# Kernel tuning notes

Hardware: AMD Instinct MI355X
Metric: run time of the kernel (lower is better)

Reference implementation:

```python
import jax, jax.numpy as jnp
import numpy as np

D_MODEL = 1024
N_HEADS = 16
HEAD_DIM = D_MODEL // N_HEADS


def setup_inputs() -> dict:
    key = jax.random.key(0)
    ks = jax.random.split(key, 9)
    s = 1.0 / np.sqrt(D_MODEL)
    inp = {
        "x": jax.random.normal(ks[0], (4, 2048, D_MODEL), dtype=jnp.float32),
        "wq": jax.random.uniform(ks[1], (D_MODEL, D_MODEL), jnp.float32, -s, s),
        "bq": jax.random.uniform(ks[2], (D_MODEL,), jnp.float32, -s, s),
        "wk": jax.random.uniform(ks[3], (D_MODEL, D_MODEL), jnp.float32, -s, s),
        "bk": jax.random.uniform(ks[4], (D_MODEL,), jnp.float32, -s, s),
        "wv": jax.random.uniform(ks[5], (D_MODEL, D_MODEL), jnp.float32, -s, s),
        "bv": jax.random.uniform(ks[6], (D_MODEL,), jnp.float32, -s, s),
        "wo": jax.random.uniform(ks[7], (D_MODEL, D_MODEL), jnp.float32, -s, s),
        "bo": jax.random.uniform(ks[8], (D_MODEL,), jnp.float32, -s, s),
    }
    return inp


def reference(x, wq, bq, wk, bk, wv, bv, wo, bo):
    b, s, d = x.shape
    h, hd = N_HEADS, HEAD_DIM
    # projections (torch Linear: y = x @ W.T + b; here weights stored as [in, out])
    q = (x @ wq + bq).reshape(b, s, h, hd).transpose(0, 2, 1, 3)  # [b,h,s,hd]
    k = (x @ wk + bk).reshape(b, s, h, hd).transpose(0, 2, 1, 3)
    v = (x @ wv + bv).reshape(b, s, h, hd).transpose(0, 2, 1, 3)
    scores = jnp.einsum("bhqd,bhkd->bhqk", q, k) / jnp.sqrt(jnp.float32(hd))
    causal = jnp.tril(jnp.ones((s, s), dtype=bool))
    scores = jnp.where(causal, scores, -jnp.inf)
    weights = jax.nn.softmax(scores, axis=-1)
    attn = jnp.einsum("bhqk,bhkd->bhqd", weights, v)  # [b,h,s,hd]
    attn = attn.transpose(0, 2, 1, 3).reshape(b, s, d)
    return attn @ wo + bo
```

## Files before the change

kernel.cpp:

```cpp
#include <hip/hip_runtime.h>
#include <cstddef>

#define D_MODEL 1024
#define NH 16
#define HD 64
#define BATCH 4
#define SEQ 2048
#define MTOT (BATCH * SEQ)

typedef _Float16 half8 __attribute__((ext_vector_type(8)));
typedef _Float16 half4v __attribute__((ext_vector_type(4)));
typedef float f32x4 __attribute__((ext_vector_type(4)));

#if __has_builtin(__builtin_amdgcn_exp2f)
#define EXP2(x) __builtin_amdgcn_exp2f(x)
#else
#define EXP2(x) __expf((x)*0.69314718056f)
#endif

#define ASYNC_COPY16(g, l)                                                    \
    __builtin_amdgcn_global_load_lds(                                         \
        (__attribute__((address_space(1))) const void*)(g),                   \
        (__attribute__((address_space(3))) void*)(l), 16, 0, 0)

#define LDSFRAG(S, R, CH)                                                     \
    (*(const half8*)((const char*)(S) + ((R) << 7) +                          \
                     ((((CH) << 1)) ^ (((R) & 7) << 4))))
#define LDSWADDR(S, R, CH)                                                    \
    ((half8*)((char*)(S) + ((R) << 7) + ((((CH) << 1)) ^ (((R) & 7) << 4))))

__global__ __launch_bounds__(256) void prep(
    const float* __restrict__ x, _Float16* __restrict__ xh,
    const float* __restrict__ W0, const float* __restrict__ W1,
    const float* __restrict__ W2, const float* __restrict__ W3,
    _Float16* __restrict__ T0, _Float16* __restrict__ T1,
    _Float16* __restrict__ T2, _Float16* __restrict__ T3)
{
    __shared__ float T[64][65];
    const int bid = blockIdx.x;
    if (bid < 256) {
        const size_t base = (size_t)bid * 4096 + threadIdx.x;
#pragma unroll
        for (int it = 0; it < 16; ++it) {
            const size_t i = base + (size_t)it * 256;
            const float4* p = (const float4*)x + 2 * i;
            float4 a = p[0], b = p[1];
            half8 h;
            h[0] = (_Float16)a.x; h[1] = (_Float16)a.y; h[2] = (_Float16)a.z; h[3] = (_Float16)a.w;
            h[4] = (_Float16)b.x; h[5] = (_Float16)b.y; h[6] = (_Float16)b.z; h[7] = (_Float16)b.w;
            *((half8*)xh + i) = h;
        }
    } else {
        const int t = bid - 256;
        const int mtx = t >> 8;
        const float* W = (mtx == 0) ? W0 : (mtx == 1) ? W1 : (mtx == 2) ? W2 : W3;
        _Float16*   Wt = (mtx == 0) ? T0 : (mtx == 1) ? T1 : (mtx == 2) ? T2 : T3;
        const int tile = t & 255;
        const int k0 = (tile >> 4) * 64, n0 = (tile & 15) * 64;
        const int r = threadIdx.x >> 4, c4 = (threadIdx.x & 15) * 4;

#pragma unroll
        for (int i = 0; i < 4; ++i) {
            float4 v = *(const float4*)(W + (size_t)(k0 + r + 16 * i) * 1024 + n0 + c4);
            T[r + 16 * i][c4 + 0] = v.x; T[r + 16 * i][c4 + 1] = v.y;
            T[r + 16 * i][c4 + 2] = v.z; T[r + 16 * i][c4 + 3] = v.w;
        }
        __syncthreads();
#pragma unroll
        for (int i = 0; i < 4; ++i) {
            const int n = r + 16 * i;
            half4v h;
            h[0] = (_Float16)T[c4 + 0][n]; h[1] = (_Float16)T[c4 + 1][n];
            h[2] = (_Float16)T[c4 + 2][n]; h[3] = (_Float16)T[c4 + 3][n];
            *(half4v*)(Wt + (size_t)(n0 + n) * 1024 + k0 + c4) = h;
        }
    }
}

template <int QKV>
__global__ __launch_bounds__(256) void gemm_mfma(
    const _Float16* __restrict__ A,
    const _Float16* __restrict__ Bt0, const _Float16* __restrict__ Bt1, const _Float16* __restrict__ Bt2,
    const float* __restrict__ bi0, const float* __restrict__ bi1, const float* __restrict__ bi2,
    void* __restrict__ C0, void* __restrict__ C1, void* __restrict__ C2)
{
    const int L = blockIdx.x;
    const int y = L & 63;
    const int c_ = L >> 6;
    const int z  = QKV ? (c_ >> 3) : 0;
    const int xb = QKV ? (c_ & 7) : c_;

    const _Float16* Bt = (z == 0) ? Bt0 : (z == 1) ? Bt1 : Bt2;
    const float*   bia = (z == 0) ? bi0 : (z == 1) ? bi1 : bi2;
    void*            C = (z == 0) ? C0  : (z == 1) ? C1  : C2;

    __shared__ _Float16 As[128][64];
    __shared__ _Float16 Bs[128][64];

    const int tid  = threadIdx.x;
    const int w    = tid >> 6;
    const int lane = tid & 63;
    const int l15  = lane & 15;
    const int lg   = lane >> 4;
    const int m0 = y * 128;
    const int n0 = xb * 128;
    const int wm = (w >> 1) * 64, wn = (w & 1) * 64;

    const int rsub = lane >> 3;
    const int cswz = ((lane & 7) ^ rsub) * 8;

    const _Float16* gA = A  + (size_t)(m0 + 32 * w + rsub) * 1024 + cswz;
    const _Float16* gB = Bt + (size_t)(n0 + 32 * w + rsub) * 1024 + cswz;
    char* lA = (char*)As + (size_t)(w * 4) * 1024;
    char* lB = (char*)Bs + (size_t)(w * 4) * 1024;

    f32x4 acc[4][4];
#pragma unroll
    for (int i = 0; i < 4; ++i)
#pragma unroll
        for (int j = 0; j < 4; ++j) { acc[i][j][0] = 0.f; acc[i][j][1] = 0.f; acc[i][j][2] = 0.f; acc[i][j][3] = 0.f; }

    for (int kt = 0; kt < 16; ++kt) {
        const int k0 = kt * 64;
        __syncthreads();
#pragma unroll
        for (int i = 0; i < 4; ++i) {
            ASYNC_COPY16(gA + (size_t)(8 * i) * 1024 + k0, lA + i * 1024);
            ASYNC_COPY16(gB + (size_t)(8 * i) * 1024 + k0, lB + i * 1024);
        }
        __syncthreads();

#pragma unroll
        for (int c = 0; c < 2; ++c) {
            half8 af[4], bf[4];
#pragma unroll
            for (int i = 0; i < 4; ++i) af[i] = LDSFRAG(As, wm + 16 * i + l15, 32 * c + 8 * lg);
#pragma unroll
            for (int j = 0; j < 4; ++j) bf[j] = LDSFRAG(Bs, wn + 16 * j + l15, 32 * c + 8 * lg);
#pragma unroll
            for (int i = 0; i < 4; ++i)
#pragma unroll
                for (int j = 0; j < 4; ++j)
                    acc[i][j] = __builtin_amdgcn_mfma_f32_16x16x32_f16(af[i], bf[j], acc[i][j], 0, 0, 0);
        }
    }

    float bvv[4];
#pragma unroll
    for (int j = 0; j < 4; ++j) bvv[j] = bia[n0 + wn + 16 * j + l15];

#pragma unroll
    for (int i = 0; i < 4; ++i)
#pragma unroll
        for (int j = 0; j < 4; ++j)
#pragma unroll
            for (int r = 0; r < 4; ++r) {
                const int m = m0 + wm + 16 * i + 4 * lg + r;
                const int n = n0 + wn + 16 * j + l15;
                const float val = acc[i][j][r] + bvv[j];
                if (QKV) {
                    const int bb = m >> 11, ss = m & 2047, hh = n >> 6, hd = n & 63;
                    if (z < 2)
                        ((_Float16*)C)[((size_t)(bb * NH + hh) * SEQ + ss) * HD + hd] = (_Float16)val;
                    else
                        ((_Float16*)C)[((size_t)(bb * NH + hh) * HD + hd) * SEQ + ss] = (_Float16)val;
                } else {
                    ((float*)C)[(size_t)m * 1024 + n] = val;
                }
            }
}

__global__ __launch_bounds__(256, 6) void attn_fwd_mfma(
    const _Float16* __restrict__ Q, const _Float16* __restrict__ K,
    const _Float16* __restrict__ Vt, _Float16* __restrict__ O)
{
    __shared__ _Float16 Ks[64][64];
    __shared__ _Float16 Vs[64][64];
    __shared__ _Float16 Ps[4][16][72];

    const int tid  = threadIdx.x;
    const int w    = tid >> 6;
    const int lane = tid & 63;
    const int l15  = lane & 15;
    const int lg   = lane >> 4;

    const int bid = blockIdx.x;
    const int bh  = bid & 63;
    const int qtb = bid >> 6;
    const int b  = bh >> 4, h = bh & 15;

    const _Float16* Qb  = Q  + (size_t)bh * SEQ * HD;
    const _Float16* Kb  = K  + (size_t)bh * SEQ * HD;
    const _Float16* Vtb = Vt + (size_t)bh * HD * SEQ;

    const int srow = tid >> 3;
    const int scol = (tid & 7) * 8;

    for (int pass = 0; pass < 2; ++pass) {
        const int qt = pass ? qtb : (31 - qtb);
        const int q0 = qt * 64;
        const int ntiles = qt + 1;

        half8 qa[2];
        {
            const _Float16* qp = Qb + (size_t)(q0 + 16 * w + l15) * HD + 8 * lg;
            qa[0] = *(const half8*)(qp);
            qa[1] = *(const half8*)(qp + 32);
#pragma unroll
            for (int c = 0; c < 2; ++c)
#pragma unroll
                for (int j = 0; j < 8; ++j)
                    qa[c][j] = (_Float16)((float)qa[c][j] * 0.18033688f);
        }

        f32x4 o_[4];
#pragma unroll
        for (int ft = 0; ft < 4; ++ft) { o_[ft][0] = 0.f; o_[ft][1] = 0.f; o_[ft][2] = 0.f; o_[ft][3] = 0.f; }
        float lp_t = 0.f;

        half8 kreg[2], vreg[2];
#pragma unroll
        for (int j = 0; j < 2; ++j) {
            kreg[j] = *(const half8*)(Kb  + (size_t)(srow + 32 * j) * HD + scol);
            vreg[j] = *(const half8*)(Vtb + (size_t)(srow + 32 * j) * SEQ + scol);
        }

        for (int kt = 0; kt < ntiles; ++kt) {
            __syncthreads();
#pragma unroll
            for (int j = 0; j < 2; ++j) {
                const int row = srow + 32 * j;
                *LDSWADDR(Ks, row, scol) = kreg[j];
                *LDSWADDR(Vs, row, scol) = vreg[j];
            }
            __syncthreads();

            if (kt + 1 < ntiles) {
                const int k0 = (kt + 1) * 64;
#pragma unroll
                for (int j = 0; j < 2; ++j) {
                    kreg[j] = *(const half8*)(Kb  + (size_t)(k0 + srow + 32 * j) * HD + scol);
                    vreg[j] = *(const half8*)(Vtb + (size_t)(srow + 32 * j) * SEQ + k0 + scol);
                }
            }

            f32x4 s[4];
#pragma unroll
            for (int f = 0; f < 4; ++f) { s[f][0] = 0.f; s[f][1] = 0.f; s[f][2] = 0.f; s[f][3] = 0.f; }
#pragma unroll
            for (int c = 0; c < 2; ++c)
#pragma unroll
                for (int f = 0; f < 4; ++f) {
                    half8 kb = LDSFRAG(Ks, 16 * f + l15, 32 * c + 8 * lg);
                    s[f] = __builtin_amdgcn_mfma_f32_16x16x32_f16(kb, qa[c], s[f], 0, 0, 0);
                }

            const bool dg = (kt == qt);
#pragma unroll
            for (int f = 0; f < 4; ++f) {
                half4v ph;
#pragma unroll
                for (int r = 0; r < 4; ++r) {
                    float p = EXP2(s[f][r]);
                    if (dg && (16 * f + 4 * lg + r > 16 * w + l15)) p = 0.f;
                    lp_t += p;
                    ph[r] = (_Float16)p;
                }
                *(half4v*)&Ps[w][l15][16 * f + 4 * lg] = ph;
            }

            half8 pa[2];
            pa[0] = *(const half8*)&Ps[w][l15][8 * lg];
            pa[1] = *(const half8*)&Ps[w][l15][32 + 8 * lg];
#pragma unroll
            for (int c = 0; c < 2; ++c)
#pragma unroll
                for (int ft = 0; ft < 4; ++ft) {
                    half8 vb = LDSFRAG(Vs, 16 * ft + l15, 32 * c + 8 * lg);
                    o_[ft] = __builtin_amdgcn_mfma_f32_16x16x32_f16(pa[c], vb, o_[ft], 0, 0, 0);
                }
        }

        float rs = lp_t;
        rs += __shfl_xor(rs, 16);
        rs += __shfl_xor(rs, 32);
#pragma unroll
        for (int r = 0; r < 4; ++r) {
            const float inv = 1.0f / __shfl(rs, 4 * lg + r, 64);
            _Float16* orow = O + (size_t)(b * SEQ + q0 + 16 * w + 4 * lg + r) * D_MODEL + h * HD + l15;
#pragma unroll
            for (int ft = 0; ft < 4; ++ft) orow[16 * ft] = (_Float16)(o_[ft][r] * inv);
        }
        __syncthreads();
    }
}

extern "C" void kernel_launch(void* const* d_in, const int* in_sizes, int n_in,
                              void* d_out, int out_size, void* d_ws, size_t ws_size,
                              hipStream_t stream)
{
    const float* x  = (const float*)d_in[0];
    const float* wq = (const float*)d_in[1];
    const float* bq = (const float*)d_in[2];
    const float* wk = (const float*)d_in[3];
    const float* bk = (const float*)d_in[4];
    const float* wv = (const float*)d_in[5];
    const float* bv = (const float*)d_in[6];
    const float* wo = (const float*)d_in[7];
    const float* bo = (const float*)d_in[8];
    float* out = (float*)d_out;

    const size_t SZ = (size_t)MTOT * D_MODEL;
    const size_t WZ = (size_t)D_MODEL * D_MODEL;

    _Float16* xh  = (_Float16*)d_ws;
    _Float16* wtq = xh + SZ;
    _Float16* wtk = wtq + WZ;
    _Float16* wtv = wtk + WZ;
    _Float16* wto = wtv + WZ;
    _Float16* Qh  = wto + WZ;
    _Float16* Kh  = Qh + SZ;
    _Float16* Vtg = Kh + SZ;
    _Float16* AOh = Vtg + SZ;

    prep<<<dim3(1280), 256, 0, stream>>>(x, xh, wq, wk, wv, wo, wtq, wtk, wtv, wto);
    gemm_mfma<1><<<dim3(1536), 256, 0, stream>>>(xh, wtq, wtk, wtv, bq, bk, bv, Qh, Kh, Vtg);
    attn_fwd_mfma<<<dim3(1024), 256, 0, stream>>>(Qh, Kh, Vtg, AOh);
    gemm_mfma<0><<<dim3(512), 256, 0, stream>>>(AOh, wto, wto, wto, bo, bo, bo, out, out, out);
}
```

Measured before the change: 268.9 us.

## Double attention query tile to 128 rows per block for K/V reuse

Each attention block now processes 128 query rows (two 16-row sub-tiles per wave) instead of 64, so every K/V tile loaded into LDS is reused by twice as many queries. The grid is halved to 512 blocks and launch bounds lowered to 4 to accommodate doubled accumulator registers. This reduces K/V global/LDS traffic and syncs per query but lowers occupancy, halves the number of blocks, and adds wasted masked work on the two diagonal tiles.

```diff
diff --git a/kernel.cpp b/kernel.cpp
--- a/kernel.cpp
+++ b/kernel.cpp
@@ -170,13 +170,13 @@
             }
 }
 
-__global__ __launch_bounds__(256, 6) void attn_fwd_mfma(
+__global__ __launch_bounds__(256, 4) void attn_fwd_mfma(
     const _Float16* __restrict__ Q, const _Float16* __restrict__ K,
     const _Float16* __restrict__ Vt, _Float16* __restrict__ O)
 {
     __shared__ _Float16 Ks[64][64];
     __shared__ _Float16 Vs[64][64];
-    __shared__ _Float16 Ps[4][16][72];
+    __shared__ _Float16 Ps[8][16][72];
 
     const int tid  = threadIdx.x;
     const int w    = tid >> 6;
@@ -197,26 +197,29 @@
     const int scol = (tid & 7) * 8;
 
     for (int pass = 0; pass < 2; ++pass) {
-        const int qt = pass ? qtb : (31 - qtb);
-        const int q0 = qt * 64;
-        const int ntiles = qt + 1;
-
-        half8 qa[2];
-        {
-            const _Float16* qp = Qb + (size_t)(q0 + 16 * w + l15) * HD + 8 * lg;
-            qa[0] = *(const half8*)(qp);
-            qa[1] = *(const half8*)(qp + 32);
+        const int qt = pass ? qtb : (15 - qtb);
+        const int q0 = qt * 128;
+        const int ntiles = 2 * qt + 2;
+
+        half8 qa[2][2];
+#pragma unroll
+        for (int u = 0; u < 2; ++u) {
+            const _Float16* qp = Qb + (size_t)(q0 + 16 * (2 * w + u) + l15) * HD + 8 * lg;
+            qa[u][0] = *(const half8*)(qp);
+            qa[u][1] = *(const half8*)(qp + 32);
 #pragma unroll
             for (int c = 0; c < 2; ++c)
 #pragma unroll
                 for (int j = 0; j < 8; ++j)
-                    qa[c][j] = (_Float16)((float)qa[c][j] * 0.18033688f);
-        }
-
-        f32x4 o_[4];
-#pragma unroll
-        for (int ft = 0; ft < 4; ++ft) { o_[ft][0] = 0.f; o_[ft][1] = 0.f; o_[ft][2] = 0.f; o_[ft][3] = 0.f; }
-        float lp_t = 0.f;
+                    qa[u][c][j] = (_Float16)((float)qa[u][c][j] * 0.18033688f);
+        }
+
+        f32x4 o_[2][4];
+#pragma unroll
+        for (int u = 0; u < 2; ++u)
+#pragma unroll
+            for (int ft = 0; ft < 4; ++ft) { o_[u][ft][0] = 0.f; o_[u][ft][1] = 0.f; o_[u][ft][2] = 0.f; o_[u][ft][3] = 0.f; }
+        float lp_t[2] = {0.f, 0.f};
 
         half8 kreg[2], vreg[2];
 #pragma unroll
@@ -244,52 +247,67 @@
                 }
             }
 
-            f32x4 s[4];
-#pragma unroll
-            for (int f = 0; f < 4; ++f) { s[f][0] = 0.f; s[f][1] = 0.f; s[f][2] = 0.f; s[f][3] = 0.f; }
+            f32x4 s0[4], s1[4];
+#pragma unroll
+            for (int f = 0; f < 4; ++f) {
+                s0[f][0] = 0.f; s0[f][1] = 0.f; s0[f][2] = 0.f; s0[f][3] = 0.f;
+                s1[f][0] = 0.f; s1[f][1] = 0.f; s1[f][2] = 0.f; s1[f][3] = 0.f;
+            }
 #pragma unroll
             for (int c = 0; c < 2; ++c)
 #pragma unroll
                 for (int f = 0; f < 4; ++f) {
                     half8 kb = LDSFRAG(Ks, 16 * f + l15, 32 * c + 8 * lg);
-                    s[f] = __builtin_amdgcn_mfma_f32_16x16x32_f16(kb, qa[c], s[f], 0, 0, 0);
-                }
-
-            const bool dg = (kt == qt);
-#pragma unroll
-            for (int f = 0; f < 4; ++f) {
-                half4v ph;
-#pragma unroll
-                for (int r = 0; r < 4; ++r) {
-                    float p = EXP2(s[f][r]);
-                    if (dg && (16 * f + 4 * lg + r > 16 * w + l15)) p = 0.f;
-                    lp_t += p;
-                    ph[r] = (_Float16)p;
-                }
-                *(half4v*)&Ps[w][l15][16 * f + 4 * lg] = ph;
-            }
-
-            half8 pa[2];
-            pa[0] = *(const half8*)&Ps[w][l15][8 * lg];
-            pa[1] = *(const half8*)&Ps[w][l15][32 + 8 * lg];
+                    s0[f] = __builtin_amdgcn_mfma_f32_16x16x32_f16(kb, qa[0][c], s0[f], 0, 0, 0);
+                    s1[f] = __builtin_amdgcn_mfma_f32_16x16x32_f16(kb, qa[1][c], s1[f], 0, 0, 0);
+                }
+
+            const bool dg = (kt >= 2 * qt);
+#pragma unroll
+            for (int u = 0; u < 2; ++u) {
+                const int qg = q0 + 16 * (2 * w + u) + l15;
+#pragma unroll
+                for (int f = 0; f < 4; ++f) {
+                    half4v ph;
+#pragma unroll
+                    for (int r = 0; r < 4; ++r) {
+                        const float sv = (u == 0) ? s0[f][r] : s1[f][r];
+                        float p = EXP2(sv);
+                        if (dg && (kt * 64 + 16 * f + 4 * lg + r > qg)) p = 0.f;
+                        lp_t[u] += p;
+                        ph[r] = (_Float16)p;
+                    }
+                    *(half4v*)&Ps[2 * w + u][l15][16 * f + 4 * lg] = ph;
+                }
+            }
+
+            half8 pa0[2], pa1[2];
+            pa0[0] = *(const half8*)&Ps[2 * w][l15][8 * lg];
+            pa0[1] = *(const half8*)&Ps[2 * w][l15][32 + 8 * lg];
+            pa1[0] = *(const half8*)&Ps[2 * w + 1][l15][8 * lg];
+            pa1[1] = *(const half8*)&Ps[2 * w + 1][l15][32 + 8 * lg];
 #pragma unroll
             for (int c = 0; c < 2; ++c)
 #pragma unroll
                 for (int ft = 0; ft < 4; ++ft) {
                     half8 vb = LDSFRAG(Vs, 16 * ft + l15, 32 * c + 8 * lg);
-                    o_[ft] = __builtin_amdgcn_mfma_f32_16x16x32_f16(pa[c], vb, o_[ft], 0, 0, 0);
-                }
-        }
-
-        float rs = lp_t;
-        rs += __shfl_xor(rs, 16);
-        rs += __shfl_xor(rs, 32);
-#pragma unroll
-        for (int r = 0; r < 4; ++r) {
-            const float inv = 1.0f / __shfl(rs, 4 * lg + r, 64);
-            _Float16* orow = O + (size_t)(b * SEQ + q0 + 16 * w + 4 * lg + r) * D_MODEL + h * HD + l15;
-#pragma unroll
-            for (int ft = 0; ft < 4; ++ft) orow[16 * ft] = (_Float16)(o_[ft][r] * inv);
+                    o_[0][ft] = __builtin_amdgcn_mfma_f32_16x16x32_f16(pa0[c], vb, o_[0][ft], 0, 0, 0);
+                    o_[1][ft] = __builtin_amdgcn_mfma_f32_16x16x32_f16(pa1[c], vb, o_[1][ft], 0, 0, 0);
+                }
+        }
+
+#pragma unroll
+        for (int u = 0; u < 2; ++u) {
+            float rs = lp_t[u];
+            rs += __shfl_xor(rs, 16);
+            rs += __shfl_xor(rs, 32);
+#pragma unroll
+            for (int r = 0; r < 4; ++r) {
+                const float inv = 1.0f / __shfl(rs, 4 * lg + r, 64);
+                _Float16* orow = O + (size_t)(b * SEQ + q0 + 16 * (2 * w + u) + 4 * lg + r) * D_MODEL + h * HD + l15;
+#pragma unroll
+                for (int ft = 0; ft < 4; ++ft) orow[16 * ft] = (_Float16)(o_[u][ft][r] * inv);
+            }
         }
         __syncthreads();
     }
@@ -325,6 +343,6 @@
 
     prep<<<dim3(1280), 256, 0, stream>>>(x, xh, wq, wk, wv, wo, wtq, wtk, wtv, wto);
     gemm_mfma<1><<<dim3(1536), 256, 0, stream>>>(xh, wtq, wtk, wtv, bq, bk, bv, Qh, Kh, Vtg);
-    attn_fwd_mfma<<<dim3(1024), 256, 0, stream>>>(Qh, Kh, Vtg, AOh);
+    attn_fwd_mfma<<<dim3(512), 256, 0, stream>>>(Qh, Kh, Vtg, AOh);
     gemm_mfma<0><<<dim3(512), 256, 0, stream>>>(AOh, wto, wto, wto, bo, bo, bo, out, out, out);
 }
```

Measured after the change: 298.1 us. +10.9%, slower.
